# Optimization experiments

Measured on AMD Instinct MI355X. Metric: run time of the kernel, lower is better.

The kernel has to match this reference:

```python
import jax, jax.numpy as jnp
import numpy as np

D_MODEL = 2048
NUM_HEADS = 16
D_K = D_MODEL // NUM_HEADS  # 128, per-head dim used for RoPE
ROPE_THETA = 10000.0
MAX_SEQ_LEN = 2048
BATCH = 4
SEQ = 2048


def _trunc_normal(key, shape, std):
    # approximate trunc_normal_(mean=0, std, a=-3std, b=3std)
    return jnp.clip(std * jax.random.normal(key, shape), -3 * std, 3 * std)


def setup_inputs() -> dict:
    key = jax.random.key(0)
    ks = jax.random.split(key, 6)
    x = jax.random.normal(ks[0], (BATCH, SEQ, D_MODEL), dtype=jnp.float32)
    token_positions = jnp.arange(SEQ, dtype=jnp.int32)
    std = float(np.sqrt(2.0 / (D_MODEL + D_MODEL)))
    wq = _trunc_normal(ks[1], (D_MODEL, D_MODEL), std)  # (d_out, d_in)
    wk = _trunc_normal(ks[2], (D_MODEL, D_MODEL), std)
    wv = _trunc_normal(ks[3], (D_MODEL, D_MODEL), std)
    wo = _trunc_normal(ks[4], (D_MODEL, D_MODEL), std)
    return {"x": x, "token_positions": token_positions,
            "wq": wq, "wk": wk, "wv": wv, "wo": wo}


def _rope(t, pos):
    # t: (b, h, n, d_k), pos: (n,) int
    # interleaved pairs: (x1, x2) = (t[..., 0::2], t[..., 1::2])
    freqs = 1.0 / (ROPE_THETA ** (jnp.arange(0, D_K, 2, dtype=jnp.float32) / D_K))
    angles = pos.astype(jnp.float32)[:, None] * freqs[None, :]  # (n, d_k/2)
    cos = jnp.cos(angles).astype(t.dtype)
    sin = jnp.sin(angles).astype(t.dtype)
    tr = t.reshape(*t.shape[:-1], D_K // 2, 2)
    x1, x2 = tr[..., 0], tr[..., 1]
    y1 = cos * x1 - sin * x2
    y2 = sin * x1 + cos * x2
    return jnp.stack([y1, y2], axis=-1).reshape(t.shape)


def reference(x, token_positions, wq, wk, wv, wo):
    b, n, d = x.shape
    q = jnp.einsum('bnd,od->bno', x, wq)
    k = jnp.einsum('bnd,od->bno', x, wk)
    v = jnp.einsum('bnd,od->bno', x, wv)
    # split heads for RoPE: (b, n, h*dk) -> (b, h, n, dk)
    split = lambda t: t.reshape(b, n, NUM_HEADS, D_K).transpose(0, 2, 1, 3)
    merge = lambda t: t.transpose(0, 2, 1, 3).reshape(b, n, d)
    q = merge(_rope(split(q), token_positions))
    k = merge(_rope(split(k), token_positions))
    # NOTE: source merges heads back BEFORE flash attention -> single-head
    # attention over full d_model with causal mask, scale 1/sqrt(d_model)
    scale = 1.0 / jnp.sqrt(jnp.asarray(d, dtype=x.dtype))
    scores = jnp.einsum('bqd,bkd->bqk', q, k) * scale  # (b, n, n)
    causal = jnp.tril(jnp.ones((n, n), dtype=bool))
    scores = jnp.where(causal[None, :, :], scores, jnp.finfo(scores.dtype).min)
    attn = jax.nn.softmax(scores, axis=-1)
    out = jnp.einsum('bqk,bkd->bqd', attn, v)
    return jnp.einsum('bnd,od->bno', out, wo)
```

## Files before the change

kernel.cpp:

```cpp
#include <hip/hip_runtime.h>
#include <hip/hip_bf16.h>
#include <cstdint>
#include <cmath>

typedef __attribute__((ext_vector_type(4))) float f32x4;
typedef __attribute__((ext_vector_type(8))) short bf16x8;

#define BAR()   __builtin_amdgcn_s_barrier()
#define PRIO1() __builtin_amdgcn_s_setprio(1)
#define PRIO0() __builtin_amdgcn_s_setprio(0)
#define WAITV4() asm volatile("s_waitcnt vmcnt(4)" ::: "memory")
#define WAITV0() asm volatile("s_waitcnt vmcnt(0)" ::: "memory")
#define MM(a,b,c) __builtin_amdgcn_mfma_f32_16x16x32_bf16((a),(b),(c),0,0,0)

__device__ __forceinline__ void gl_lds16(const __hip_bfloat16* g, char* l) {
    __builtin_amdgcn_global_load_lds(
        (const __attribute__((address_space(1))) void*)g,
        (__attribute__((address_space(3))) void*)l, 16, 0, 0);
}
__device__ __forceinline__ void store_c(float* C, size_t i, float v) { C[i] = v; }
__device__ __forceinline__ void store_c(__hip_bfloat16* C, size_t i, float v) { C[i] = __float2bfloat16(v); }

#define STAGEA(nb, kt) do{ gl_lds16(Asrc + (kt),                        lds + (nb)         + wb); \
                           gl_lds16(Asrc + (size_t)128 * lda + (kt),    lds + (nb) +  8192 + wb);}while(0)
#define STAGEB(nb, kt) do{ gl_lds16(Bsrc + (kt),                        lds + (nb) + 16384 + wb); \
                           gl_lds16(Bsrc + (size_t)128 * ldb + (kt),    lds + (nb) + 24576 + wb);}while(0)

template<typename CT, int MODE>
__global__ __launch_bounds__(512, 2)
void gemm256(const __hip_bfloat16* __restrict__ A, const __hip_bfloat16* __restrict__ B,
             CT* __restrict__ C, int K, int lda, int ldb, int ldc, int nbx,
             float alpha, size_t sA, size_t sB, size_t sC)
{
    __shared__ __align__(1024) char lds[98304];

    int bm0, bn0;
    if (MODE == 1) {
        const int wg = blockIdx.x;
        int by = (int)((sqrtf(8.f * wg + 1.f) - 1.f) * 0.5f);
        if (by * (by + 1) / 2 > wg) --by;
        if ((by + 1) * (by + 2) / 2 <= wg) ++by;
        const int bx = wg - by * (by + 1) / 2;
        bm0 = by * 256; bn0 = bx * 256;
    } else if (MODE == 2) {
        const int g = blockIdx.x;
        const int nby = gridDim.x / nbx;
        const int bx = g % nbx;
        const int by = (g / nbx + bx) % nby;
        bm0 = by * 256; bn0 = bx * 256;
    } else {
        const int nwg = gridDim.x;
        const int q8 = nwg >> 3, r8 = nwg & 7;
        const int xcd = blockIdx.x & 7, blk = blockIdx.x >> 3;
        const int wg = (xcd < r8 ? xcd * (q8 + 1) : r8 * (q8 + 1) + (xcd - r8) * q8) + blk;
        bm0 = (wg / nbx) * 256; bn0 = (wg % nbx) * 256;
    }

    A += sA * blockIdx.y; B += sB * blockIdx.y; C += sC * blockIdx.y;

    const int tid  = threadIdx.x;
    const int lane = tid & 63;
    const int w    = tid >> 6;
    const int wb   = w * 1024;

    const int rb   = (lane & 15) * 64 + (lane >> 4) * 16;
    const int rswz = rb ^ (((rb >> 9) & 1) << 5);
    const int srA  = (w >> 2) * 8;
    const int srB  = (w & 3) * 4;

    const int q0 = tid * 16;
    const int uq = q0 ^ (((q0 >> 9) & 1) << 5);
    const int r0 = ((q0 >> 10) << 4) | ((uq >> 6) & 15);
    const int c0 = (uq & 63) >> 1;
    const __hip_bfloat16* Asrc = A + (size_t)(bm0 + r0) * lda + c0;
    const __hip_bfloat16* Bsrc = B + (size_t)(bn0 + r0) * ldb + c0;

    f32x4 acc[8][4] = {};
    bf16x8 af[4], bf[4];

    const int klim = bm0 + 256;
    const int kend = (MODE == 2) ? (K < klim ? K : klim) : K;
    const int nt   = kend >> 5;

    STAGEA(0, 0); STAGEB(0, 0);
    if (nt > 1) { STAGEA(32768, 32); STAGEB(32768, 32); }

    for (int t = 0; t < nt; ++t) {
        if (t + 1 < nt) WAITV4(); else WAITV0();
        BAR();
        const char* dA = lds + (t % 3) * 32768;
        const char* dB = dA + 16384;
        const int  nbo = ((t + 2) % 3) * 32768;
        const bool pf  = (t + 2 < nt);
        const int  kt  = (t + 2) << 5;

#pragma unroll
        for (int i = 0; i < 4; ++i) af[i] = *(const bf16x8*)(dA + ((srA + i) << 10) + rswz);
#pragma unroll
        for (int i = 0; i < 4; ++i) bf[i] = *(const bf16x8*)(dB + ((srB + i) << 10) + rswz);
        if (pf) STAGEA(nbo, kt);
        BAR();
        PRIO1();
#pragma unroll
        for (int mi = 0; mi < 4; ++mi)
#pragma unroll
            for (int ni = 0; ni < 4; ++ni)
                acc[mi][ni] = MM(af[mi], bf[ni], acc[mi][ni]);
        PRIO0();

#pragma unroll
        for (int i = 0; i < 4; ++i) af[i] = *(const bf16x8*)(dA + ((srA + 4 + i) << 10) + rswz);
        if (pf) STAGEB(nbo, kt);
        BAR();
        PRIO1();
#pragma unroll
        for (int mi = 0; mi < 4; ++mi)
#pragma unroll
            for (int ni = 0; ni < 4; ++ni)
                acc[4 + mi][ni] = MM(af[mi], bf[ni], acc[4 + mi][ni]);
        PRIO0();
    }

    const int cr = (lane >> 4) * 4, cc = lane & 15;
    const int wrow = bm0 + (w >> 2) * 128, wcol = bn0 + (w & 3) * 64;
#pragma unroll
    for (int mi = 0; mi < 8; ++mi)
#pragma unroll
        for (int ni = 0; ni < 4; ++ni) {
            const int row = wrow + mi * 16 + cr;
            const int col = wcol + ni * 16 + cc;
#pragma unroll
            for (int j = 0; j < 4; ++j)
                store_c(C, (size_t)(row + j) * ldc + col, acc[mi][ni][j] * alpha);
        }
}

__global__ void f32_to_bf16_vec(const float* __restrict__ in,
                                __hip_bfloat16* __restrict__ out, int n4)
{
    int i = blockIdx.x * 256 + threadIdx.x;
    if (i >= n4) return;
    float4 v = ((const float4*)in)[i];
    union { ushort4 u; __hip_bfloat16 h[4]; } o;
    o.h[0] = __float2bfloat16(v.x);
    o.h[1] = __float2bfloat16(v.y);
    o.h[2] = __float2bfloat16(v.z);
    o.h[3] = __float2bfloat16(v.w);
    ((ushort4*)out)[i] = o.u;
}

__global__ void conv_w4(const float* __restrict__ w0, const float* __restrict__ w1,
                        const float* __restrict__ w2, const float* __restrict__ w3,
                        __hip_bfloat16* o0, __hip_bfloat16* o1,
                        __hip_bfloat16* o2, __hip_bfloat16* o3, int n4)
{
    int i = blockIdx.x * 256 + threadIdx.x;
    if (i >= n4) return;
    const float* src; __hip_bfloat16* dst;
    switch (blockIdx.y) {
        case 0: src = w0; dst = o0; break;
        case 1: src = w1; dst = o1; break;
        case 2: src = w2; dst = o2; break;
        default: src = w3; dst = o3; break;
    }
    float4 v = ((const float4*)src)[i];
    union { ushort4 u; __hip_bfloat16 h[4]; } o;
    o.h[0] = __float2bfloat16(v.x);
    o.h[1] = __float2bfloat16(v.y);
    o.h[2] = __float2bfloat16(v.z);
    o.h[3] = __float2bfloat16(v.w);
    ((ushort4*)dst)[i] = o.u;
}

__global__ void rope_table(const int* __restrict__ pos, float2* __restrict__ tab, int N)
{
    int i = blockIdx.x * 256 + threadIdx.x;
    if (i >= N * 64) return;
    int n = i >> 6, j = i & 63;
    float p = (float)pos[n];
    float ang = p * powf(10000.f, -(float)j * (1.0f / 64.0f));
    tab[i] = make_float2(cosf(ang), sinf(ang));
}

__global__ void rope_apply2(__hip_bfloat16* __restrict__ Q, __hip_bfloat16* __restrict__ K,
                            const float2* __restrict__ tab)
{
    int i = blockIdx.x * 256 + threadIdx.x;
    __hip_bfloat16* T = blockIdx.y ? K : Q;
    int r  = i >> 8;
    int cb = (i & 255) << 3;
    int n  = r & 2047;
    int j0 = (cb >> 1) & 63;
    union { bf16x8 v; __hip_bfloat162 h[4]; } u;
    __hip_bfloat16* p = T + ((size_t)r << 11) + cb;
    u.v = *(const bf16x8*)p;
#pragma unroll
    for (int k = 0; k < 4; ++k) {
        float2 cs = tab[(n << 6) + j0 + k];
        float x1 = __bfloat162float(u.h[k].x);
        float x2 = __bfloat162float(u.h[k].y);
        u.h[k].x = __float2bfloat16(cs.x * x1 - cs.y * x2);
        u.h[k].y = __float2bfloat16(cs.y * x1 + cs.x * x2);
    }
    *(bf16x8*)p = u.v;
}

__global__ void softmax_causal_ip(float* __restrict__ S, int N)
{
    const int q = blockIdx.x;
    float* srow = S + ((size_t)blockIdx.y * N + q) * N;
    __shared__ float buf[2048];
    __shared__ float red[8];
    const int tid = threadIdx.x;

    float4* b4 = (float4*)buf;
    const float4* s4 = (const float4*)srow;
    for (int i = tid; i < N / 4; i += 256) b4[i] = s4[i];
    __syncthreads();

    float m = -1e30f;
    for (int j = tid; j <= q; j += 256) m = fmaxf(m, buf[j]);
#pragma unroll
    for (int o = 32; o > 0; o >>= 1) m = fmaxf(m, __shfl_xor(m, o));
    if ((tid & 63) == 0) red[tid >> 6] = m;
    __syncthreads();
    m = fmaxf(fmaxf(red[0], red[1]), fmaxf(red[2], red[3]));

    float sum = 0.f;
    for (int j = tid; j <= q; j += 256) { float e = __expf(buf[j] - m); buf[j] = e; sum += e; }
#pragma unroll
    for (int o = 32; o > 0; o >>= 1) sum += __shfl_xor(sum, o);
    if ((tid & 63) == 0) red[4 + (tid >> 6)] = sum;
    __syncthreads();
    const float inv = 1.f / (red[4] + red[5] + red[6] + red[7]);

    __hip_bfloat162* p2 = (__hip_bfloat162*)srow;
    for (int i = tid; i < N / 2; i += 256) {
        int j0 = i * 2;
        __hip_bfloat162 h;
        h.x = __float2bfloat16(j0     <= q ? buf[j0]     * inv : 0.f);
        h.y = __float2bfloat16(j0 + 1 <= q ? buf[j0 + 1] * inv : 0.f);
        p2[i] = h;
    }
}

__global__ void transpose_bf16(const __hip_bfloat16* __restrict__ V,
                               __hip_bfloat16* __restrict__ Vt, int N)
{
    __shared__ __hip_bfloat16 tile[32][33];
    const size_t bo = (size_t)blockIdx.z * N * N;
    const int k0 = blockIdx.x * 32, d0 = blockIdx.y * 32;
    const int tx = threadIdx.x, ty = threadIdx.y;
#pragma unroll
    for (int j = 0; j < 4; ++j)
        tile[ty + 8 * j][tx] = V[bo + (size_t)(k0 + ty + 8 * j) * N + d0 + tx];
    __syncthreads();
#pragma unroll
    for (int j = 0; j < 4; ++j)
        Vt[bo + (size_t)(d0 + ty + 8 * j) * N + k0 + tx] = tile[tx][ty + 8 * j];
}

extern "C" void kernel_launch(void* const* d_in, const int* in_sizes, int n_in,
                              void* d_out, int out_size, void* d_ws, size_t ws_size,
                              hipStream_t stream)
{
    const float* x  = (const float*)d_in[0];
    const int* pos  = (const int*)d_in[1];
    const float* wq = (const float*)d_in[2];
    const float* wk = (const float*)d_in[3];
    const float* wv = (const float*)d_in[4];
    const float* wo = (const float*)d_in[5];
    float* out = (float*)d_out;

    const int B = 4, N = 2048, D = 2048;
    const int M = B * N;
    const size_t MB = 1ull << 20;
    if (ws_size < 192 * MB) return;

    char* w = (char*)d_ws;
    __hip_bfloat16* Qb  = (__hip_bfloat16*)(w + 0 * MB);
    __hip_bfloat16* Kb  = (__hip_bfloat16*)(w + 32 * MB);
    __hip_bfloat16* Vb  = (__hip_bfloat16*)(w + 64 * MB);
    __hip_bfloat16* wqb = (__hip_bfloat16*)(w + 96 * MB);
    __hip_bfloat16* wkb = (__hip_bfloat16*)(w + 104 * MB);
    __hip_bfloat16* wvb = (__hip_bfloat16*)(w + 112 * MB);
    __hip_bfloat16* wob = (__hip_bfloat16*)(w + 120 * MB);
    __hip_bfloat16* xb  = (__hip_bfloat16*)(w + 128 * MB);
    __hip_bfloat16* Vt  = xb;
    __hip_bfloat16* AO  = (__hip_bfloat16*)(w + 160 * MB);
    float2*         tab = (float2*)(w + 190 * MB);

    float* Sal = (float*)d_out;

    f32_to_bf16_vec<<<(M * D / 4 + 255) / 256, 256, 0, stream>>>(x, xb, M * D / 4);
    conv_w4<<<dim3((D * D / 4 + 255) / 256, 4), 256, 0, stream>>>(
        wq, wk, wv, wo, wqb, wkb, wvb, wob, D * D / 4);
    rope_table<<<(N * 64 + 255) / 256, 256, 0, stream>>>(pos, tab, N);

    const int nbxP = D / 256;
    dim3 gp((D / 256) * (M / 256), 1);
    gemm256<__hip_bfloat16, 0><<<gp, 512, 0, stream>>>(xb, wqb, Qb, D, D, D, D, nbxP, 1.f, 0, 0, 0);
    gemm256<__hip_bfloat16, 0><<<gp, 512, 0, stream>>>(xb, wkb, Kb, D, D, D, D, nbxP, 1.f, 0, 0, 0);
    gemm256<__hip_bfloat16, 0><<<gp, 512, 0, stream>>>(xb, wvb, Vb, D, D, D, D, nbxP, 1.f, 0, 0, 0);

    rope_apply2<<<dim3(M * 256 / 256, 2), 256, 0, stream>>>(Qb, Kb, tab);

    transpose_bf16<<<dim3(N / 32, N / 32, B), dim3(32, 8), 0, stream>>>(Vb, Vt, N);

    const float scale = 1.0f / sqrtf((float)D);
    const int nbxA = N / 256;
    const int ntri = nbxA * (nbxA + 1) / 2;
    gemm256<float, 1><<<dim3(ntri, B), 512, 0, stream>>>(
        Qb, Kb, Sal, D, D, D, N, nbxA, scale, (size_t)N * D, (size_t)N * D, (size_t)N * N);
    softmax_causal_ip<<<dim3(N, B), 256, 0, stream>>>(Sal, N);
    gemm256<__hip_bfloat16, 2><<<dim3(nbxA * nbxA, B), 512, 0, stream>>>(
        (const __hip_bfloat16*)Sal, Vt, AO, N, 2 * N, D, D, nbxA, 1.f,
        (size_t)2 * N * N, (size_t)N * D, (size_t)N * D);

    gemm256<float, 0><<<gp, 512, 0, stream>>>(AO, wob, out, D, D, D, D, nbxP, 1.f, 0, 0, 0);
}
```

Baseline: 479.6 us.

## Add 128x256 tile GEMM for Q/K projections and attention GEMMs

Introduces a gemm128 kernel with 128x256 output tiles, a smaller LDS footprint and occupancy of 4 blocks per CU, each iteration staging three 16-byte loads per thread. It is used for the Q and K projections, the causal QK^T (finer triangular tiling with 72 tiles per batch) and the PV GEMM with causal K truncation. The V and output projections keep the 256x256 kernel, which loses its mode variants. The finer triangular tiling should waste less work on masked regions and improve load balance, at the cost of less operand reuse per tile.

```diff
diff --git a/kernel.cpp b/kernel.cpp
--- a/kernel.cpp
+++ b/kernel.cpp
@@ -10,6 +10,7 @@
 #define PRIO1() __builtin_amdgcn_s_setprio(1)
 #define PRIO0() __builtin_amdgcn_s_setprio(0)
 #define WAITV4() asm volatile("s_waitcnt vmcnt(4)" ::: "memory")
+#define WAITV3() asm volatile("s_waitcnt vmcnt(3)" ::: "memory")
 #define WAITV0() asm volatile("s_waitcnt vmcnt(0)" ::: "memory")
 #define MM(a,b,c) __builtin_amdgcn_mfma_f32_16x16x32_bf16((a),(b),(c),0,0,0)
 
@@ -26,7 +27,7 @@
 #define STAGEB(nb, kt) do{ gl_lds16(Bsrc + (kt),                        lds + (nb) + 16384 + wb); \
                            gl_lds16(Bsrc + (size_t)128 * ldb + (kt),    lds + (nb) + 24576 + wb);}while(0)
 
-template<typename CT, int MODE>
+template<typename CT>
 __global__ __launch_bounds__(512, 2)
 void gemm256(const __hip_bfloat16* __restrict__ A, const __hip_bfloat16* __restrict__ B,
              CT* __restrict__ C, int K, int lda, int ldb, int ldc, int nbx,
@@ -34,27 +35,11 @@
 {
     __shared__ __align__(1024) char lds[98304];
 
-    int bm0, bn0;
-    if (MODE == 1) {
-        const int wg = blockIdx.x;
-        int by = (int)((sqrtf(8.f * wg + 1.f) - 1.f) * 0.5f);
-        if (by * (by + 1) / 2 > wg) --by;
-        if ((by + 1) * (by + 2) / 2 <= wg) ++by;
-        const int bx = wg - by * (by + 1) / 2;
-        bm0 = by * 256; bn0 = bx * 256;
-    } else if (MODE == 2) {
-        const int g = blockIdx.x;
-        const int nby = gridDim.x / nbx;
-        const int bx = g % nbx;
-        const int by = (g / nbx + bx) % nby;
-        bm0 = by * 256; bn0 = bx * 256;
-    } else {
-        const int nwg = gridDim.x;
-        const int q8 = nwg >> 3, r8 = nwg & 7;
-        const int xcd = blockIdx.x & 7, blk = blockIdx.x >> 3;
-        const int wg = (xcd < r8 ? xcd * (q8 + 1) : r8 * (q8 + 1) + (xcd - r8) * q8) + blk;
-        bm0 = (wg / nbx) * 256; bn0 = (wg % nbx) * 256;
-    }
+    const int nwg = gridDim.x;
+    const int q8 = nwg >> 3, r8 = nwg & 7;
+    const int xcd = blockIdx.x & 7, blk = blockIdx.x >> 3;
+    const int wg = (xcd < r8 ? xcd * (q8 + 1) : r8 * (q8 + 1) + (xcd - r8) * q8) + blk;
+    const int bm0 = (wg / nbx) * 256, bn0 = (wg % nbx) * 256;
 
     A += sA * blockIdx.y; B += sB * blockIdx.y; C += sC * blockIdx.y;
 
@@ -78,9 +63,7 @@
     f32x4 acc[8][4] = {};
     bf16x8 af[4], bf[4];
 
-    const int klim = bm0 + 256;
-    const int kend = (MODE == 2) ? (K < klim ? K : klim) : K;
-    const int nt   = kend >> 5;
+    const int nt = K >> 5;
 
     STAGEA(0, 0); STAGEB(0, 0);
     if (nt > 1) { STAGEA(32768, 32); STAGEB(32768, 32); }
@@ -125,6 +108,104 @@
     const int wrow = bm0 + (w >> 2) * 128, wcol = bn0 + (w & 3) * 64;
 #pragma unroll
     for (int mi = 0; mi < 8; ++mi)
+#pragma unroll
+        for (int ni = 0; ni < 4; ++ni) {
+            const int row = wrow + mi * 16 + cr;
+            const int col = wcol + ni * 16 + cc;
+#pragma unroll
+            for (int j = 0; j < 4; ++j)
+                store_c(C, (size_t)(row + j) * ldc + col, acc[mi][ni][j] * alpha);
+        }
+}
+
+#define STG128(buf, kt) do{ \
+    gl_lds16(Asrc + (kt),  lds + (buf) * 24576 +         w * 1024); \
+    gl_lds16(Bsrc0 + (kt), lds + (buf) * 24576 +  8192 + w * 1024); \
+    gl_lds16(Bsrc1 + (kt), lds + (buf) * 24576 + 16384 + w * 1024); }while(0)
+
+template<typename CT, int MODE>
+__global__ __launch_bounds__(512, 4)
+void gemm128(const __hip_bfloat16* __restrict__ A, const __hip_bfloat16* __restrict__ B,
+             CT* __restrict__ C, int K, int lda, int ldb, int ldc, int nbx,
+             float alpha, size_t sA, size_t sB, size_t sC)
+{
+    __shared__ __align__(1024) char lds[73728];
+
+    int bm0, bn0;
+    if (MODE == 1) {
+        int g = blockIdx.x, r = 0;
+        while (g >= (r >> 1) + 1) { g -= (r >> 1) + 1; ++r; }
+        bm0 = r << 7; bn0 = g << 8;
+    } else if (MODE == 2) {
+        const int g = blockIdx.x;
+        const int nby = gridDim.x / nbx;
+        const int bx = g % nbx;
+        const int by = (g / nbx + bx) % nby;
+        bm0 = by << 7; bn0 = bx << 8;
+    } else {
+        const int nwg = gridDim.x;
+        const int q8 = nwg >> 3, r8 = nwg & 7;
+        const int xcd = blockIdx.x & 7, blk = blockIdx.x >> 3;
+        const int wg = (xcd < r8 ? xcd * (q8 + 1) : r8 * (q8 + 1) + (xcd - r8) * q8) + blk;
+        bm0 = (wg / nbx) << 7; bn0 = (wg % nbx) << 8;
+    }
+
+    A += sA * blockIdx.y; B += sB * blockIdx.y; C += sC * blockIdx.y;
+
+    const int tid  = threadIdx.x;
+    const int lane = tid & 63;
+    const int w    = tid >> 6;
+
+    const int rb   = (lane & 15) * 64 + (lane >> 4) * 16;
+    const int rswz = rb ^ (((rb >> 9) & 1) << 5);
+    const int stA  = (w >> 2) * 4;
+    const int stB  = (w & 3) * 4;
+
+    const int qA  = tid * 16;
+    const int uqA = qA ^ (((qA >> 9) & 1) << 5);
+    const int rA  = ((qA >> 10) << 4) | ((uqA >> 6) & 15);
+    const int cA  = (uqA & 63) >> 1;
+    const int qB1  = 8192 + tid * 16;
+    const int uqB1 = qB1 ^ (((qB1 >> 9) & 1) << 5);
+    const int rB1  = ((qB1 >> 10) << 4) | ((uqB1 >> 6) & 15);
+    const int cB1  = (uqB1 & 63) >> 1;
+    const __hip_bfloat16* Asrc  = A + (size_t)(bm0 + rA) * lda + cA;
+    const __hip_bfloat16* Bsrc0 = B + (size_t)(bn0 + rA) * ldb + cA;
+    const __hip_bfloat16* Bsrc1 = B + (size_t)(bn0 + rB1) * ldb + cB1;
+
+    f32x4 acc[4][4] = {};
+    bf16x8 af[4], bf[4];
+
+    const int klim = bm0 + 128;
+    const int kend = (MODE == 2) ? (K < klim ? K : klim) : K;
+    const int nt   = kend >> 5;
+
+    STG128(0, 0);
+    if (nt > 1) STG128(1, 32);
+
+    for (int t = 0; t < nt; ++t) {
+        if (t + 1 < nt) WAITV3(); else WAITV0();
+        BAR();
+        const char* dA = lds + (t % 3) * 24576;
+        const char* dB = dA + 8192;
+#pragma unroll
+        for (int i = 0; i < 4; ++i) af[i] = *(const bf16x8*)(dA + ((stA + i) << 10) + rswz);
+#pragma unroll
+        for (int i = 0; i < 4; ++i) bf[i] = *(const bf16x8*)(dB + ((stB + i) << 10) + rswz);
+        if (t + 2 < nt) STG128((t + 2) % 3, (t + 2) << 5);
+        PRIO1();
+#pragma unroll
+        for (int mi = 0; mi < 4; ++mi)
+#pragma unroll
+            for (int ni = 0; ni < 4; ++ni)
+                acc[mi][ni] = MM(af[mi], bf[ni], acc[mi][ni]);
+        PRIO0();
+    }
+
+    const int cr = (lane >> 4) * 4, cc = lane & 15;
+    const int wrow = bm0 + (w >> 2) * 64, wcol = bn0 + (w & 3) * 64;
+#pragma unroll
+    for (int mi = 0; mi < 4; ++mi)
 #pragma unroll
         for (int ni = 0; ni < 4; ++ni) {
             const int row = wrow + mi * 16 + cr;
@@ -297,25 +378,25 @@
         wq, wk, wv, wo, wqb, wkb, wvb, wob, D * D / 4);
     rope_table<<<(N * 64 + 255) / 256, 256, 0, stream>>>(pos, tab, N);
 
-    const int nbxP = D / 256;
-    dim3 gp((D / 256) * (M / 256), 1);
-    gemm256<__hip_bfloat16, 0><<<gp, 512, 0, stream>>>(xb, wqb, Qb, D, D, D, D, nbxP, 1.f, 0, 0, 0);
-    gemm256<__hip_bfloat16, 0><<<gp, 512, 0, stream>>>(xb, wkb, Kb, D, D, D, D, nbxP, 1.f, 0, 0, 0);
-    gemm256<__hip_bfloat16, 0><<<gp, 512, 0, stream>>>(xb, wvb, Vb, D, D, D, D, nbxP, 1.f, 0, 0, 0);
+    gemm128<__hip_bfloat16, 0><<<dim3((D / 256) * (M / 128)), 512, 0, stream>>>(
+        xb, wqb, Qb, D, D, D, D, D / 256, 1.f, 0, 0, 0);
+    gemm128<__hip_bfloat16, 0><<<dim3((D / 256) * (M / 128)), 512, 0, stream>>>(
+        xb, wkb, Kb, D, D, D, D, D / 256, 1.f, 0, 0, 0);
+    gemm256<__hip_bfloat16><<<dim3((D / 256) * (M / 256)), 512, 0, stream>>>(
+        xb, wvb, Vb, D, D, D, D, D / 256, 1.f, 0, 0, 0);
 
     rope_apply2<<<dim3(M * 256 / 256, 2), 256, 0, stream>>>(Qb, Kb, tab);
 
     transpose_bf16<<<dim3(N / 32, N / 32, B), dim3(32, 8), 0, stream>>>(Vb, Vt, N);
 
     const float scale = 1.0f / sqrtf((float)D);
-    const int nbxA = N / 256;
-    const int ntri = nbxA * (nbxA + 1) / 2;
-    gemm256<float, 1><<<dim3(ntri, B), 512, 0, stream>>>(
-        Qb, Kb, Sal, D, D, D, N, nbxA, scale, (size_t)N * D, (size_t)N * D, (size_t)N * N);
+    gemm128<float, 1><<<dim3(72, B), 512, 0, stream>>>(
+        Qb, Kb, Sal, D, D, D, N, N / 256, scale, (size_t)N * D, (size_t)N * D, (size_t)N * N);
     softmax_causal_ip<<<dim3(N, B), 256, 0, stream>>>(Sal, N);
-    gemm256<__hip_bfloat16, 2><<<dim3(nbxA * nbxA, B), 512, 0, stream>>>(
-        (const __hip_bfloat16*)Sal, Vt, AO, N, 2 * N, D, D, nbxA, 1.f,
+    gemm128<__hip_bfloat16, 2><<<dim3((N / 128) * (N / 256), B), 512, 0, stream>>>(
+        (const __hip_bfloat16*)Sal, Vt, AO, N, 2 * N, D, D, N / 256, 1.f,
         (size_t)2 * N * N, (size_t)N * D, (size_t)N * D);
 
-    gemm256<float, 0><<<gp, 512, 0, stream>>>(AO, wob, out, D, D, D, D, nbxP, 1.f, 0, 0, 0);
-}
+    gemm256<float><<<dim3((D / 256) * (M / 256)), 512, 0, stream>>>(
+        AO, wob, out, D, D, D, D, D / 256, 1.f, 0, 0, 0);
+}
```

After: 493.8 us. 3.0% more time.

## Fuse QKV projections into one 8-phase pipelined GEMM and trim causal softmax

Applied to the files above, without the earlier changes.

Concatenates the Q, K and V weights into a single 6144-wide matrix and computes all three projections with one new 256x256 GEMM kernel (gemm8p). That kernel uses 128KB of double-buffered LDS and splits each K-step into four MFMA phases, with loads for the next tiles interleaved between them. Downstream kernels (rope, V transpose, the QK^T GEMM) take the strided QKV layout through new leading-dimension parameters. The causal softmax now reads only up to the diagonal and writes only up to the 256-column tile edge the next GEMM consumes. This aims to remove launch overhead and repeated reads of x, and to cut wasted softmax traffic, at the cost of strided Q/K/V access and more complex pipeline code.

```diff
diff --git a/kernel.cpp b/kernel.cpp
--- a/kernel.cpp
+++ b/kernel.cpp
@@ -9,6 +9,7 @@
 #define BAR()   __builtin_amdgcn_s_barrier()
 #define PRIO1() __builtin_amdgcn_s_setprio(1)
 #define PRIO0() __builtin_amdgcn_s_setprio(0)
+#define WAITV6() asm volatile("s_waitcnt vmcnt(6)" ::: "memory")
 #define WAITV4() asm volatile("s_waitcnt vmcnt(4)" ::: "memory")
 #define WAITV0() asm volatile("s_waitcnt vmcnt(0)" ::: "memory")
 #define MM(a,b,c) __builtin_amdgcn_mfma_f32_16x16x32_bf16((a),(b),(c),0,0,0)
@@ -20,6 +21,156 @@
 }
 __device__ __forceinline__ void store_c(float* C, size_t i, float v) { C[i] = v; }
 __device__ __forceinline__ void store_c(__hip_bfloat16* C, size_t i, float v) { C[i] = __float2bfloat16(v); }
+
+#define SGA8(dd, h, i, kt) do{ const int s_ = (h)*16 + (i)*8 + w; \
+    gl_lds16(Asb + (size_t)((s_>>1)<<4) * lda + ((s_&1)<<5) + (kt), \
+             lds + (dd)*65536 + (s_<<10)); }while(0)
+#define SGB8N(dd, g, kt) do{ const int sB_ = (g)*8 + w; \
+    const int hi_ = sB_ >> 4, r_ = sB_ & 15; \
+    const int wc_ = r_ >> 2, ni_ = hi_*2 + ((r_>>1)&1), kk_ = r_ & 1; \
+    gl_lds16(Bsb + (size_t)(wc_*64 + ni_*16) * ldb + (kk_<<5) + (kt), \
+             lds + (dd)*65536 + 32768 + (sB_<<10)); }while(0)
+#define LDA8(dd, miA, kk) (*(const bf16x8*)(lds + (dd)*65536 + ((sbA + (miA)*2 + (kk)) << 10) + rswz))
+#define LDB8N(dd, ni, kk) (*(const bf16x8*)(lds + (dd)*65536 + 32768 + \
+    ((((((ni)>>1)<<4) + ((w&3)<<2) + (((ni)&1)<<1) + (kk))) << 10) + rswz))
+
+template<typename CT>
+__global__ __launch_bounds__(512, 2)
+void gemm8p(const __hip_bfloat16* __restrict__ A, const __hip_bfloat16* __restrict__ B,
+            CT* __restrict__ C, int K, int lda, int ldb, int ldc, int nbx, float alpha)
+{
+    __shared__ __align__(1024) char lds[131072];
+
+    const int nwg = gridDim.x;
+    const int q8 = nwg >> 3, r8 = nwg & 7;
+    const int xcd = blockIdx.x & 7, blk = blockIdx.x >> 3;
+    const int wg = (xcd < r8 ? xcd * (q8 + 1) : r8 * (q8 + 1) + (xcd - r8) * q8) + blk;
+    const int bm0 = (wg / nbx) * 256, bn0 = (wg % nbx) * 256;
+
+    const int tid  = threadIdx.x;
+    const int lane = tid & 63;
+    const int w    = tid >> 6;
+
+    const int rb   = (lane & 15) * 64 + (lane >> 4) * 16;
+    const int rswz = rb ^ (((rb >> 9) & 1) << 5);
+    const int sbA  = (w >> 2) * 16;
+
+    const int l16 = lane * 16;
+    const int uqs = l16 ^ (((l16 >> 9) & 1) << 5);
+    const int rIn = uqs >> 6;
+    const int cIn = (uqs & 63) >> 1;
+    const __hip_bfloat16* Asb = A + (size_t)(bm0 + rIn) * lda + cIn;
+    const __hip_bfloat16* Bsb = B + (size_t)(bn0 + rIn) * ldb + cIn;
+
+    f32x4 acc[8][4] = {};
+    bf16x8 afA[4][2], bfB[2][2];
+
+    const int nt = K >> 6;
+
+    SGA8(0, 0, 0, 0); SGA8(0, 1, 0, 0);
+    SGB8N(0, 0, 0);   SGB8N(0, 1, 0);
+    SGB8N(0, 2, 0);   SGB8N(0, 3, 0);
+    SGA8(0, 0, 1, 0); SGA8(0, 1, 1, 0);
+    if (nt > 1) {
+        SGA8(1, 0, 0, 64); SGA8(1, 1, 0, 64);
+        SGB8N(1, 2, 64);   SGB8N(1, 3, 64);
+        SGA8(1, 0, 1, 64); SGA8(1, 1, 1, 64);
+        WAITV6();
+    } else WAITV0();
+    BAR();
+
+    for (int t = 0; t < nt; ++t) {
+        const int d   = t & 1, e = d ^ 1;
+        const bool p1 = (t + 1) < nt;
+        const bool p2 = (t + 2) < nt;
+        const int kt1 = (t + 1) << 6;
+        const int kt2 = (t + 2) << 6;
+
+#pragma unroll
+        for (int mi = 0; mi < 4; ++mi) { afA[mi][0] = LDA8(d, mi, 0); afA[mi][1] = LDA8(d, mi, 1); }
+#pragma unroll
+        for (int ni = 0; ni < 2; ++ni) { bfB[ni][0] = LDB8N(d, ni, 0); bfB[ni][1] = LDB8N(d, ni, 1); }
+        if (p1) { SGB8N(e, 0, kt1); SGB8N(e, 1, kt1); }
+        BAR();
+        PRIO1();
+#pragma unroll
+        for (int mi = 0; mi < 4; ++mi)
+#pragma unroll
+            for (int ni = 0; ni < 2; ++ni) {
+                f32x4 c = acc[mi][ni];
+                c = MM(afA[mi][0], bfB[ni][0], c);
+                c = MM(afA[mi][1], bfB[ni][1], c);
+                acc[mi][ni] = c;
+            }
+        PRIO0();
+        BAR();
+
+#pragma unroll
+        for (int ni = 0; ni < 2; ++ni) { bfB[ni][0] = LDB8N(d, 2 + ni, 0); bfB[ni][1] = LDB8N(d, 2 + ni, 1); }
+        if (p2) { SGA8(d, 0, 0, kt2); SGA8(d, 1, 0, kt2); }
+        BAR();
+        PRIO1();
+#pragma unroll
+        for (int mi = 0; mi < 4; ++mi)
+#pragma unroll
+            for (int ni = 0; ni < 2; ++ni) {
+                f32x4 c = acc[mi][2 + ni];
+                c = MM(afA[mi][0], bfB[ni][0], c);
+                c = MM(afA[mi][1], bfB[ni][1], c);
+                acc[mi][2 + ni] = c;
+            }
+        PRIO0();
+        BAR();
+
+#pragma unroll
+        for (int mi = 0; mi < 4; ++mi) { afA[mi][0] = LDA8(d, 4 + mi, 0); afA[mi][1] = LDA8(d, 4 + mi, 1); }
+        if (p2) { SGB8N(d, 2, kt2); SGB8N(d, 3, kt2); }
+        BAR();
+        PRIO1();
+#pragma unroll
+        for (int mi = 0; mi < 4; ++mi)
+#pragma unroll
+            for (int ni = 0; ni < 2; ++ni) {
+                f32x4 c = acc[4 + mi][2 + ni];
+                c = MM(afA[mi][0], bfB[ni][0], c);
+                c = MM(afA[mi][1], bfB[ni][1], c);
+                acc[4 + mi][2 + ni] = c;
+            }
+        PRIO0();
+        BAR();
+
+#pragma unroll
+        for (int ni = 0; ni < 2; ++ni) { bfB[ni][0] = LDB8N(d, ni, 0); bfB[ni][1] = LDB8N(d, ni, 1); }
+        if (p2) { SGA8(d, 0, 1, kt2); SGA8(d, 1, 1, kt2); WAITV6(); }
+        else WAITV0();
+        BAR();
+        PRIO1();
+#pragma unroll
+        for (int mi = 0; mi < 4; ++mi)
+#pragma unroll
+            for (int ni = 0; ni < 2; ++ni) {
+                f32x4 c = acc[4 + mi][ni];
+                c = MM(afA[mi][0], bfB[ni][0], c);
+                c = MM(afA[mi][1], bfB[ni][1], c);
+                acc[4 + mi][ni] = c;
+            }
+        PRIO0();
+        BAR();
+    }
+
+    const int cr = (lane >> 4) * 4, cc = lane & 15;
+    const int wrow = bm0 + (w >> 2) * 128, wcol = bn0 + (w & 3) * 64;
+#pragma unroll
+    for (int mi = 0; mi < 8; ++mi)
+#pragma unroll
+        for (int ni = 0; ni < 4; ++ni) {
+            const int row = wrow + mi * 16 + cr;
+            const int col = wcol + ni * 16 + cc;
+#pragma unroll
+            for (int j = 0; j < 4; ++j)
+                store_c(C, (size_t)(row + j) * ldc + col, acc[mi][ni][j] * alpha);
+        }
+}
 
 #define STAGEA(nb, kt) do{ gl_lds16(Asrc + (kt),                        lds + (nb)         + wb); \
                            gl_lds16(Asrc + (size_t)128 * lda + (kt),    lds + (nb) +  8192 + wb);}while(0)
@@ -36,11 +187,11 @@
 
     int bm0, bn0;
     if (MODE == 1) {
-        const int wg = blockIdx.x;
-        int by = (int)((sqrtf(8.f * wg + 1.f) - 1.f) * 0.5f);
-        if (by * (by + 1) / 2 > wg) --by;
-        if ((by + 1) * (by + 2) / 2 <= wg) ++by;
-        const int bx = wg - by * (by + 1) / 2;
+        const int wgi = blockIdx.x;
+        int by = (int)((sqrtf(8.f * wgi + 1.f) - 1.f) * 0.5f);
+        if (by * (by + 1) / 2 > wgi) --by;
+        if ((by + 1) * (by + 2) / 2 <= wgi) ++by;
+        const int bx = wgi - by * (by + 1) / 2;
         bm0 = by * 256; bn0 = bx * 256;
     } else if (MODE == 2) {
         const int g = blockIdx.x;
@@ -183,7 +334,7 @@
 }
 
 __global__ void rope_apply2(__hip_bfloat16* __restrict__ Q, __hip_bfloat16* __restrict__ K,
-                            const float2* __restrict__ tab)
+                            const float2* __restrict__ tab, int ld)
 {
     int i = blockIdx.x * 256 + threadIdx.x;
     __hip_bfloat16* T = blockIdx.y ? K : Q;
@@ -192,7 +343,7 @@
     int n  = r & 2047;
     int j0 = (cb >> 1) & 63;
     union { bf16x8 v; __hip_bfloat162 h[4]; } u;
-    __hip_bfloat16* p = T + ((size_t)r << 11) + cb;
+    __hip_bfloat16* p = T + (size_t)r * ld + cb;
     u.v = *(const bf16x8*)p;
 #pragma unroll
     for (int k = 0; k < 4; ++k) {
@@ -212,10 +363,11 @@
     __shared__ float buf[2048];
     __shared__ float red[8];
     const int tid = threadIdx.x;
+    const int wend = ((q >> 8) + 1) << 8;
 
     float4* b4 = (float4*)buf;
     const float4* s4 = (const float4*)srow;
-    for (int i = tid; i < N / 4; i += 256) b4[i] = s4[i];
+    for (int i = tid; i <= (q >> 2); i += 256) b4[i] = s4[i];
     __syncthreads();
 
     float m = -1e30f;
@@ -235,7 +387,7 @@
     const float inv = 1.f / (red[4] + red[5] + red[6] + red[7]);
 
     __hip_bfloat162* p2 = (__hip_bfloat162*)srow;
-    for (int i = tid; i < N / 2; i += 256) {
+    for (int i = tid; i < (wend >> 1); i += 256) {
         int j0 = i * 2;
         __hip_bfloat162 h;
         h.x = __float2bfloat16(j0     <= q ? buf[j0]     * inv : 0.f);
@@ -245,15 +397,16 @@
 }
 
 __global__ void transpose_bf16(const __hip_bfloat16* __restrict__ V,
-                               __hip_bfloat16* __restrict__ Vt, int N)
+                               __hip_bfloat16* __restrict__ Vt, int N, int ldv)
 {
     __shared__ __hip_bfloat16 tile[32][33];
+    const size_t bi = (size_t)blockIdx.z * N * ldv;
     const size_t bo = (size_t)blockIdx.z * N * N;
     const int k0 = blockIdx.x * 32, d0 = blockIdx.y * 32;
     const int tx = threadIdx.x, ty = threadIdx.y;
 #pragma unroll
     for (int j = 0; j < 4; ++j)
-        tile[ty + 8 * j][tx] = V[bo + (size_t)(k0 + ty + 8 * j) * N + d0 + tx];
+        tile[ty + 8 * j][tx] = V[bi + (size_t)(k0 + ty + 8 * j) * ldv + d0 + tx];
     __syncthreads();
 #pragma unroll
     for (int j = 0; j < 4; ++j)
@@ -274,48 +427,48 @@
 
     const int B = 4, N = 2048, D = 2048;
     const int M = B * N;
+    const int D3 = 3 * D;
     const size_t MB = 1ull << 20;
     if (ws_size < 192 * MB) return;
 
     char* w = (char*)d_ws;
-    __hip_bfloat16* Qb  = (__hip_bfloat16*)(w + 0 * MB);
-    __hip_bfloat16* Kb  = (__hip_bfloat16*)(w + 32 * MB);
-    __hip_bfloat16* Vb  = (__hip_bfloat16*)(w + 64 * MB);
-    __hip_bfloat16* wqb = (__hip_bfloat16*)(w + 96 * MB);
-    __hip_bfloat16* wkb = (__hip_bfloat16*)(w + 104 * MB);
-    __hip_bfloat16* wvb = (__hip_bfloat16*)(w + 112 * MB);
-    __hip_bfloat16* wob = (__hip_bfloat16*)(w + 120 * MB);
-    __hip_bfloat16* xb  = (__hip_bfloat16*)(w + 128 * MB);
-    __hip_bfloat16* Vt  = xb;
-    __hip_bfloat16* AO  = (__hip_bfloat16*)(w + 160 * MB);
-    float2*         tab = (float2*)(w + 190 * MB);
+    __hip_bfloat16* QKV  = (__hip_bfloat16*)(w + 0 * MB);
+    __hip_bfloat16* wqkv = (__hip_bfloat16*)(w + 96 * MB);
+    __hip_bfloat16* wob  = (__hip_bfloat16*)(w + 120 * MB);
+    __hip_bfloat16* xb   = (__hip_bfloat16*)(w + 128 * MB);
+    __hip_bfloat16* Vt   = xb;
+    __hip_bfloat16* AO   = (__hip_bfloat16*)(w + 160 * MB);
+    float2*         tab  = (float2*)(w + 190 * MB);
+
+    __hip_bfloat16* Qb = QKV;
+    __hip_bfloat16* Kb = QKV + D;
+    __hip_bfloat16* Vb = QKV + 2 * D;
 
     float* Sal = (float*)d_out;
 
     f32_to_bf16_vec<<<(M * D / 4 + 255) / 256, 256, 0, stream>>>(x, xb, M * D / 4);
     conv_w4<<<dim3((D * D / 4 + 255) / 256, 4), 256, 0, stream>>>(
-        wq, wk, wv, wo, wqb, wkb, wvb, wob, D * D / 4);
+        wq, wk, wv, wo, wqkv, wqkv + (size_t)D * D, wqkv + (size_t)2 * D * D, wob, D * D / 4);
     rope_table<<<(N * 64 + 255) / 256, 256, 0, stream>>>(pos, tab, N);
 
-    const int nbxP = D / 256;
-    dim3 gp((D / 256) * (M / 256), 1);
-    gemm256<__hip_bfloat16, 0><<<gp, 512, 0, stream>>>(xb, wqb, Qb, D, D, D, D, nbxP, 1.f, 0, 0, 0);
-    gemm256<__hip_bfloat16, 0><<<gp, 512, 0, stream>>>(xb, wkb, Kb, D, D, D, D, nbxP, 1.f, 0, 0, 0);
-    gemm256<__hip_bfloat16, 0><<<gp, 512, 0, stream>>>(xb, wvb, Vb, D, D, D, D, nbxP, 1.f, 0, 0, 0);
-
-    rope_apply2<<<dim3(M * 256 / 256, 2), 256, 0, stream>>>(Qb, Kb, tab);
-
-    transpose_bf16<<<dim3(N / 32, N / 32, B), dim3(32, 8), 0, stream>>>(Vb, Vt, N);
+    gemm8p<__hip_bfloat16><<<dim3((D3 / 256) * (M / 256)), 512, 0, stream>>>(
+        xb, wqkv, QKV, D, D, D, D3, D3 / 256, 1.f);
+
+    rope_apply2<<<dim3(M, 2), 256, 0, stream>>>(Qb, Kb, tab, D3);
+
+    transpose_bf16<<<dim3(N / 32, N / 32, B), dim3(32, 8), 0, stream>>>(Vb, Vt, N, D3);
 
     const float scale = 1.0f / sqrtf((float)D);
     const int nbxA = N / 256;
     const int ntri = nbxA * (nbxA + 1) / 2;
     gemm256<float, 1><<<dim3(ntri, B), 512, 0, stream>>>(
-        Qb, Kb, Sal, D, D, D, N, nbxA, scale, (size_t)N * D, (size_t)N * D, (size_t)N * N);
+        Qb, Kb, Sal, D, D3, D3, N, nbxA, scale,
+        (size_t)N * D3, (size_t)N * D3, (size_t)N * N);
     softmax_causal_ip<<<dim3(N, B), 256, 0, stream>>>(Sal, N);
     gemm256<__hip_bfloat16, 2><<<dim3(nbxA * nbxA, B), 512, 0, stream>>>(
-        (const __hip_bfloat16*)Sal, Vt, AO, N, 2 * N, D, D, nbxA, 1.f,
-        (size_t)2 * N * N, (size_t)N * D, (size_t)N * D);
-
-    gemm256<float, 0><<<gp, 512, 0, stream>>>(AO, wob, out, D, D, D, D, nbxP, 1.f, 0, 0, 0);
-}
+        (const __hip_bfloat16*)Sal, Vt, AO, N, 2 * N, N, D, nbxA, 1.f,
+        (size_t)2 * N * N, (size_t)N * N, (size_t)N * D);
+
+    gemm256<float, 0><<<dim3((D / 256) * (M / 256)), 512, 0, stream>>>(
+        AO, wob, out, D, D, D, D, D / 256, 1.f, 0, 0, 0);
+}
```

After: 463.1 us. 1.04x faster.
